# Kernel tuning notes

Measured on AMD Instinct MI355X. Metric: run time of the kernel, lower is better.

The kernel has to match this reference:

```python
import jax, jax.numpy as jnp
import numpy as np

STATE_DIM = 256
MAX_NODES = 64
EPS = 1e-5
EDGE_THRESHOLD = 0.3


def _glorot(key, shape):
    fan_in = shape[0]
    bound = 1.0 / np.sqrt(fan_in)
    return jax.random.uniform(key, shape, jnp.float32, -bound, bound)


def setup_inputs() -> dict:
    key = jax.random.key(0)
    ks = jax.random.split(key, 16)
    D = STATE_DIM
    d2, d4 = D // 2, D // 4
    inp = {
        "state_sequence": jax.random.normal(ks[0], (256, 128, D), jnp.float32),
        # node encoder
        "W1": _glorot(ks[1], (D, d2)), "b1": jnp.zeros((d2,), jnp.float32),
        "W2": _glorot(ks[2], (d2, d4)), "b2": jnp.zeros((d4,), jnp.float32),
        "gamma": jnp.ones((d4,), jnp.float32), "beta": jnp.zeros((d4,), jnp.float32),
        # edge predictor (input dim d2 = 2*d4)
        "E1": _glorot(ks[3], (d2, 64)), "bE1": jnp.zeros((64,), jnp.float32),
        "E2": _glorot(ks[4], (64, 32)), "bE2": jnp.zeros((32,), jnp.float32),
        "E3": _glorot(ks[5], (32, 1)), "bE3": jnp.zeros((1,), jnp.float32),
        # strength estimator
        "S1": _glorot(ks[6], (d2, 32)), "bS1": jnp.zeros((32,), jnp.float32),
        "S2": _glorot(ks[7], (32, 1)), "bS2": jnp.zeros((1,), jnp.float32),
    }
    return inp


def reference(state_sequence, W1, b1, W2, b2, gamma, beta,
              E1, bE1, E2, bE2, E3, bE3, S1, bS1, S2, bS2):
    B, S, D = state_sequence.shape
    N = MAX_NODES
    # pad if seq shorter than max_nodes (static shapes, here S >= N so no-op branch)
    if S < N:
        state_sequence = jnp.pad(state_sequence, ((0, 0), (0, N - S), (0, 0)))
        S = N
    # linspace indices, truncated to long like torch.linspace(..., dtype=long)
    idx = jnp.linspace(0.0, S - 1, N).astype(jnp.int32)
    nodes = state_sequence[:, idx]                      # [B, N, D]

    # node encoder: Linear -> ReLU -> (Dropout eval) -> Linear -> LayerNorm
    h = jax.nn.relu(jnp.einsum('bnd,de->bne', nodes, W1) + b1)
    h = jnp.einsum('bnd,de->bne', h, W2) + b2           # [B, N, D//4]
    mu = jnp.mean(h, axis=-1, keepdims=True)
    var = jnp.mean((h - mu) ** 2, axis=-1, keepdims=True)
    node_features = (h - mu) * jax.lax.rsqrt(var + EPS) * gamma + beta
    node_features = jnp.nan_to_num(node_features, nan=0.0)

    d4 = node_features.shape[-1]
    # pair input is concat([f_i, f_j]); split first-layer weights to avoid
    # materializing the [B,N,N,2*d4] concat tensor.
    # edge predictor first layer
    ei = jnp.einsum('bnd,dh->bnh', node_features, E1[:d4])   # [B, N, 64]
    ej = jnp.einsum('bnd,dh->bnh', node_features, E1[d4:])
    he = jax.nn.relu(ei[:, :, None, :] + ej[:, None, :, :] + bE1)  # [B,N,N,64]
    he = jax.nn.relu(jnp.einsum('bijh,hk->bijk', he, E2) + bE2)    # [B,N,N,32]
    edge_prob = jax.nn.sigmoid(jnp.einsum('bijk,ko->bijo', he, E3) + bE3)[..., 0]

    # strength estimator
    si = jnp.einsum('bnd,dh->bnh', node_features, S1[:d4])
    sj = jnp.einsum('bnd,dh->bnh', node_features, S1[d4:])
    hs = jax.nn.relu(si[:, :, None, :] + sj[:, None, :, :] + bS1)  # [B,N,N,32]
    strength = jnp.tanh(jnp.einsum('bijk,ko->bijo', hs, S2) + bS2)[..., 0]

    offdiag = 1.0 - jnp.eye(N, dtype=edge_prob.dtype)   # i != j only
    adjacency = edge_prob * offdiag
    strengths = strength * offdiag
    adjacency = jnp.where(adjacency > EDGE_THRESHOLD, adjacency, 0.0)
    return node_features, adjacency, strengths
```

## Files before the change

### kernel.cpp

```cpp
#include <hip/hip_runtime.h>
#include <hip/hip_bf16.h>
#include <math.h>

typedef __attribute__((ext_vector_type(8))) short short8;
typedef __attribute__((ext_vector_type(4))) short short4v;
typedef __attribute__((ext_vector_type(4))) float f32x4;
typedef __attribute__((ext_vector_type(2))) _Float16 h2;
typedef __attribute__((ext_vector_type(4))) _Float16 h4;
typedef __attribute__((ext_vector_type(8))) _Float16 h8;

__device__ __forceinline__ short f2bf(float f) {
    __hip_bfloat16 h = __float2bfloat16(f);
    return __builtin_bit_cast(short, h);
}

__global__ __launch_bounds__(256)
void kernelA0(const float* __restrict__ W1, const float* __restrict__ W2,
              const float* __restrict__ E1, const float* __restrict__ S1,
              short* __restrict__ wT)
{
    const int tid = blockIdx.x * 256 + threadIdx.x;
    {
        const int k = tid >> 7, n = tid & 127;
        wT[n * 256 + k] = f2bf(W1[tid]);
    }
    if (tid < 8192) {
        const int k = tid >> 6, n = tid & 63;
        wT[32768 + n * 128 + k] = f2bf(W2[tid]);
    }
    if (tid < 8192) {
        const int rr = tid >> 6, c = tid & 63;
        const int o = (rr < 64) ? c : (64 + c);
        const int k = (rr < 64) ? rr : (rr - 64);
        wT[40960 + o * 64 + k] = f2bf(E1[tid]);
    }
    if (tid < 4096) {
        const int rr = tid >> 5, c = tid & 31;
        const int o = (rr < 64) ? (128 + c) : (160 + c);
        const int k = (rr < 64) ? rr : (rr - 64);
        wT[40960 + o * 64 + k] = f2bf(S1[tid]);
    }
}

constexpr int XS_S  = 264;
constexpr int NH1_S = 136;
constexpr int NHS_S = 68;
constexpr int NNF_S = 72;

__global__ __launch_bounds__(256, 2)
void kernelN(const float* __restrict__ x,
             const float* __restrict__ b1, const float* __restrict__ b2,
             const float* __restrict__ gamma, const float* __restrict__ beta,
             const short* __restrict__ wT,
             const float* __restrict__ bE1, const float* __restrict__ bS1,
             float* __restrict__ out_nf,
             float* __restrict__ ws_ei, float* __restrict__ ws_ej,
             float* __restrict__ ws_si, float* __restrict__ ws_sj)
{
    __shared__ short Xs [16 * XS_S];
    __shared__ short h1B[16 * NH1_S];
    __shared__ float Hs [16 * NHS_S];
    __shared__ short nfB[16 * NNF_S];

    const int t  = threadIdx.x;
    const int rg = blockIdx.x;
    const int b  = blockIdx.y;
    const int w  = t >> 6, l = t & 63, g = l >> 4, r = l & 15;
    const short* W1T = wT;
    const short* W2T = wT + 32768;
    const short* WcT = wT + 40960;

    {
        const int row = t >> 4, c0 = t & 15;
        const int m = 16 * rg + row;
        const int srow = (m == 63) ? 127 : (int)((float)m * (127.0f / 63.0f));
        const float* xrow = x + ((size_t)b * 128 + srow) * 256;
#pragma unroll
        for (int i = 0; i < 4; ++i) {
            const int c4 = (c0 + 16 * i) * 4;
            const float4 v = *(const float4*)(xrow + c4);
            short4v s;
            s[0] = f2bf(v.x); s[1] = f2bf(v.y); s[2] = f2bf(v.z); s[3] = f2bf(v.w);
            *(short4v*)&Xs[row * XS_S + c4] = s;
        }
    }
    __syncthreads();

#pragma unroll
    for (int nt2 = 0; nt2 < 2; ++nt2) {
        const int n = 32 * w + 16 * nt2 + r;
        f32x4 acca = {0.f, 0.f, 0.f, 0.f};
        f32x4 accb = {0.f, 0.f, 0.f, 0.f};
#pragma unroll
        for (int ks = 0; ks < 4; ++ks) {
            const short8 a0  = *(const short8*)&Xs[r * XS_S + 32 * ks + 8 * g];
            const short8 a1  = *(const short8*)&Xs[r * XS_S + 32 * (ks + 4) + 8 * g];
            const short8 bwa = *(const short8*)(W1T + (size_t)n * 256 + 32 * ks + 8 * g);
            const short8 bwb = *(const short8*)(W1T + (size_t)n * 256 + 32 * (ks + 4) + 8 * g);
            acca = __builtin_amdgcn_mfma_f32_16x16x32_bf16(a0, bwa, acca, 0, 0, 0);
            accb = __builtin_amdgcn_mfma_f32_16x16x32_bf16(a1, bwb, accb, 0, 0, 0);
        }
        const float b1v = b1[n];
#pragma unroll
        for (int q = 0; q < 4; ++q)
            h1B[(4 * g + q) * NH1_S + n] = f2bf(fmaxf(acca[q] + accb[q] + b1v, 0.f));
    }
    __syncthreads();

    {
        const int n = 16 * w + r;
        f32x4 acca = {0.f, 0.f, 0.f, 0.f};
        f32x4 accb = {0.f, 0.f, 0.f, 0.f};
#pragma unroll
        for (int ks2 = 0; ks2 < 2; ++ks2) {
            const short8 ha0 = *(const short8*)&h1B[r * NH1_S + 32 * (2 * ks2) + 8 * g];
            const short8 ha1 = *(const short8*)&h1B[r * NH1_S + 32 * (2 * ks2 + 1) + 8 * g];
            const short8 bw0 = *(const short8*)(W2T + (size_t)n * 128 + 32 * (2 * ks2) + 8 * g);
            const short8 bw1 = *(const short8*)(W2T + (size_t)n * 128 + 32 * (2 * ks2 + 1) + 8 * g);
            acca = __builtin_amdgcn_mfma_f32_16x16x32_bf16(ha0, bw0, acca, 0, 0, 0);
            accb = __builtin_amdgcn_mfma_f32_16x16x32_bf16(ha1, bw1, accb, 0, 0, 0);
        }
        const float b2v = b2[n];
#pragma unroll
        for (int q = 0; q < 4; ++q)
            Hs[(4 * g + q) * NHS_S + n] = acca[q] + accb[q] + b2v;
    }
    __syncthreads();

    {
        const int row = t >> 4, c4 = (t & 15) * 4;
        const float4 v = *(const float4*)&Hs[row * NHS_S + c4];
        float s = v.x + v.y + v.z + v.w;
        s += __shfl_xor(s, 1); s += __shfl_xor(s, 2);
        s += __shfl_xor(s, 4); s += __shfl_xor(s, 8);
        const float mu = s * (1.0f / 64.0f);
        float vs = 0.f;
        { const float d0 = v.x-mu, d1 = v.y-mu, d2 = v.z-mu, d3 = v.w-mu;
          vs = fmaf(d0,d0, fmaf(d1,d1, fmaf(d2,d2, d3*d3))); }
        vs += __shfl_xor(vs, 1); vs += __shfl_xor(vs, 2);
        vs += __shfl_xor(vs, 4); vs += __shfl_xor(vs, 8);
        const float rstd = rsqrtf(vs * (1.0f / 64.0f) + 1e-5f);
        const float4 gv = *(const float4*)(gamma + c4);
        const float4 bv = *(const float4*)(beta  + c4);
        float4 o;
        o.x = fmaf((v.x - mu) * rstd, gv.x, bv.x);
        o.y = fmaf((v.y - mu) * rstd, gv.y, bv.y);
        o.z = fmaf((v.z - mu) * rstd, gv.z, bv.z);
        o.w = fmaf((v.w - mu) * rstd, gv.w, bv.w);
        *(float4*)(out_nf + (size_t)b * 4096 + (size_t)(16 * rg + row) * 64 + c4) = o;
        short4v ob;
        ob[0] = f2bf(o.x); ob[1] = f2bf(o.y); ob[2] = f2bf(o.z); ob[3] = f2bf(o.w);
        *(short4v*)&nfB[row * NNF_S + c4] = ob;
    }
    __syncthreads();

    const short8 na0 = *(const short8*)&nfB[r * NNF_S + 8 * g];
    const short8 na1 = *(const short8*)&nfB[r * NNF_S + 32 + 8 * g];
#pragma unroll
    for (int k3 = 0; k3 < 3; ++k3) {
        const int nt = 3 * w + k3;
        const int c = 16 * nt + r;
        const short8 bw0 = *(const short8*)(WcT + (size_t)c * 64 + 8 * g);
        const short8 bw1 = *(const short8*)(WcT + (size_t)c * 64 + 32 + 8 * g);
        f32x4 acc = {0.f, 0.f, 0.f, 0.f};
        acc = __builtin_amdgcn_mfma_f32_16x16x32_bf16(na0, bw0, acc, 0, 0, 0);
        acc = __builtin_amdgcn_mfma_f32_16x16x32_bf16(na1, bw1, acc, 0, 0, 0);
        float* dst; int cc, rs; float badd = 0.f;
        if (nt < 4)       { dst = ws_ei + (size_t)b * 4096; cc = c;       rs = 64; badd = bE1[c]; }
        else if (nt < 8)  { dst = ws_ej + (size_t)b * 4096; cc = c - 64;  rs = 64; }
        else if (nt < 10) { dst = ws_si + (size_t)b * 2048; cc = c - 128; rs = 32; badd = bS1[c - 128]; }
        else              { dst = ws_sj + (size_t)b * 2048; cc = c - 160; rs = 32; }
#pragma unroll
        for (int q = 0; q < 4; ++q)
            dst[(size_t)(16 * rg + 4 * g + q) * rs + cc] = acc[q] + badd;
    }
}

constexpr int EJH = 34;
constexpr int SJH = 18;

__global__ __launch_bounds__(256, 2)
void kernelB(const float* __restrict__ ws_ei, const float* __restrict__ ws_ej,
             const float* __restrict__ ws_si, const float* __restrict__ ws_sj,
             const float* __restrict__ E2,
             const float* __restrict__ bE2, const float* __restrict__ E3,
             const float* __restrict__ bE3,
             const float* __restrict__ S2, const float* __restrict__ bS2,
             float* __restrict__ out_adj, float* __restrict__ out_str)
{
    __shared__ h2 ejH[64 * EJH];
    __shared__ h2 eiH[16 * EJH];
    __shared__ h2 sjH[64 * SJH];
    __shared__ h2 siH[16 * SJH];
    __shared__ float bE2s[32], E3s[32];

    const int t  = threadIdx.x;
    const int qi = blockIdx.x;
    const int b  = blockIdx.y;
    const int w  = t >> 6, l = t & 63;
    const int g  = l >> 4, r = l & 15;

#pragma unroll
    for (int it = 0; it < 8; ++it) {
        const int f = t + 256 * it; const int j = f >> 5, k2 = f & 31;
        const float2 v = *(const float2*)&ws_ej[(size_t)b * 4096 + (size_t)j * 64 + 2 * k2];
        h2 p; p[0] = (_Float16)v.x; p[1] = (_Float16)v.y;
        ejH[j * EJH + k2] = p;
    }
#pragma unroll
    for (int it = 0; it < 2; ++it) {
        const int f = t + 256 * it; const int rr = f >> 5, k2 = f & 31;
        const float2 v = *(const float2*)&ws_ei[(size_t)b * 4096 + (size_t)(qi * 16 + rr) * 64 + 2 * k2];
        h2 p; p[0] = (_Float16)v.x; p[1] = (_Float16)v.y;
        eiH[rr * EJH + k2] = p;
    }
#pragma unroll
    for (int it = 0; it < 4; ++it) {
        const int f = t + 256 * it; const int j = f >> 4, k2 = f & 15;
        const float2 v = *(const float2*)&ws_sj[(size_t)b * 2048 + (size_t)j * 32 + 2 * k2];
        h2 p; p[0] = (_Float16)v.x; p[1] = (_Float16)v.y;
        sjH[j * SJH + k2] = p;
    }
    {
        const int rr = t >> 4, k2 = t & 15;
        const float2 v = *(const float2*)&ws_si[(size_t)b * 2048 + (size_t)(qi * 16 + rr) * 32 + 2 * k2];
        h2 p; p[0] = (_Float16)v.x; p[1] = (_Float16)v.y;
        siH[rr * SJH + k2] = p;
    }
    if (t < 32)      bE2s[t] = bE2[t];
    else if (t < 64) E3s[t - 32] = E3[t - 32];

    h8 aE00, aE10, aE01, aE11;
#pragma unroll
    for (int e = 0; e < 8; ++e) {
        aE00[e] = (_Float16)E2[(size_t)(8 * g + e) * 32 + r];
        aE10[e] = (_Float16)E2[(size_t)(8 * g + e + 32) * 32 + r];
        aE01[e] = (_Float16)E2[(size_t)(8 * g + e) * 32 + r + 16];
        aE11[e] = (_Float16)E2[(size_t)(8 * g + e + 32) * 32 + r + 16];
    }
    const float bE3v = bE3[0], bS2v = bS2[0];
    const h4 z4 = {(_Float16)0.f, (_Float16)0.f, (_Float16)0.f, (_Float16)0.f};
    __syncthreads();

    h4 ei0a[4], ei0b[4], ei1a[4], ei1b[4];
#pragma unroll
    for (int ii = 0; ii < 4; ++ii) {
        const int il = 4 * w + ii;
        ei0a[ii] = *(const h4*)&eiH[il * EJH + 4 * g];
        ei0b[ii] = *(const h4*)&eiH[il * EJH + 4 * g + 2];
        ei1a[ii] = *(const h4*)&eiH[il * EJH + 16 + 4 * g];
        ei1b[ii] = *(const h4*)&eiH[il * EJH + 16 + 4 * g + 2];
    }

    for (int jt = 0; jt < 4; ++jt) {
        const int j = (jt << 4) + r;
        const h4 ej0a = *(const h4*)&ejH[j * EJH + 4 * g];
        const h4 ej0b = *(const h4*)&ejH[j * EJH + 4 * g + 2];
        const h4 ej1a = *(const h4*)&ejH[j * EJH + 16 + 4 * g];
        const h4 ej1b = *(const h4*)&ejH[j * EJH + 16 + 4 * g + 2];

#pragma unroll
        for (int ii = 0; ii < 4; ++ii) {
            const int ig = qi * 16 + 4 * w + ii;

            const h4 he0a = __builtin_elementwise_max(ei0a[ii] + ej0a, z4);
            const h4 he0b = __builtin_elementwise_max(ei0b[ii] + ej0b, z4);
            const h4 he1a = __builtin_elementwise_max(ei1a[ii] + ej1a, z4);
            const h4 he1b = __builtin_elementwise_max(ei1b[ii] + ej1b, z4);
            const h8 b0 = __builtin_shufflevector(he0a, he0b, 0, 1, 2, 3, 4, 5, 6, 7);
            const h8 b1 = __builtin_shufflevector(he1a, he1b, 0, 1, 2, 3, 4, 5, 6, 7);

            f32x4 acc0 = {0.f, 0.f, 0.f, 0.f};
            f32x4 acc1 = {0.f, 0.f, 0.f, 0.f};
            acc0 = __builtin_amdgcn_mfma_f32_16x16x32_f16(aE00, b0, acc0, 0, 0, 0);
            acc0 = __builtin_amdgcn_mfma_f32_16x16x32_f16(aE10, b1, acc0, 0, 0, 0);
            acc1 = __builtin_amdgcn_mfma_f32_16x16x32_f16(aE01, b0, acc1, 0, 0, 0);
            acc1 = __builtin_amdgcn_mfma_f32_16x16x32_f16(aE11, b1, acc1, 0, 0, 0);

            float pe = 0.f;
#pragma unroll
            for (int q = 0; q < 4; ++q) {
                const int k0 = 4 * g + q;
                pe += fmaxf(acc0[q] + bE2s[k0], 0.f) * E3s[k0];
                pe += fmaxf(acc1[q] + bE2s[k0 + 16], 0.f) * E3s[k0 + 16];
            }
            pe += __shfl_xor(pe, 16);
            pe += __shfl_xor(pe, 32);

            if (l < 16) {
                const float z = pe + bE3v;
                const float p = 1.0f / (1.0f + __expf(-z));
                const float av = (j == ig || !(p > 0.3f)) ? 0.f : p;
                out_adj[(size_t)b * 4096 + (size_t)ig * 64 + j] = av;
            }
        }
    }

    {
        h4 s2h[8];
#pragma unroll
        for (int q8 = 0; q8 < 8; ++q8) {
            h4 p;
            p[0] = (_Float16)S2[4 * q8];     p[1] = (_Float16)S2[4 * q8 + 1];
            p[2] = (_Float16)S2[4 * q8 + 2]; p[3] = (_Float16)S2[4 * q8 + 3];
            s2h[q8] = p;
        }
        const int j = t & 63;
        const int ib = (t >> 6) * 4;
        h4 sj4[8];
#pragma unroll
        for (int q8 = 0; q8 < 8; ++q8)
            sj4[q8] = *(const h4*)&sjH[j * SJH + 2 * q8];
#pragma unroll
        for (int ii = 0; ii < 4; ++ii) {
            const int il = ib + ii;
            const int ig = qi * 16 + il;
            float sacc = 0.f;
#pragma unroll
            for (int q8 = 0; q8 < 8; ++q8) {
                const h4 si4 = *(const h4*)&siH[il * SJH + 2 * q8];
                const h4 hs = __builtin_elementwise_max(si4 + sj4[q8], z4);
                const h2 lo   = __builtin_shufflevector(hs, hs, 0, 1);
                const h2 hi   = __builtin_shufflevector(hs, hs, 2, 3);
                const h2 s2lo = __builtin_shufflevector(s2h[q8], s2h[q8], 0, 1);
                const h2 s2hi = __builtin_shufflevector(s2h[q8], s2h[q8], 2, 3);
                sacc = __builtin_amdgcn_fdot2(lo, s2lo, sacc, false);
                sacc = __builtin_amdgcn_fdot2(hi, s2hi, sacc, false);
            }
            const float xs = sacc + bS2v;
            const float e2x = __expf(2.0f * xs);
            const float sv = (j == ig) ? 0.f : (e2x - 1.0f) / (e2x + 1.0f);
            out_str[(size_t)b * 4096 + (size_t)ig * 64 + j] = sv;
        }
    }
}

extern "C" void kernel_launch(void* const* d_in, const int* in_sizes, int n_in,
                              void* d_out, int out_size, void* d_ws, size_t ws_size,
                              hipStream_t stream)
{
    const float* x     = (const float*)d_in[0];
    const float* W1    = (const float*)d_in[1];
    const float* b1    = (const float*)d_in[2];
    const float* W2    = (const float*)d_in[3];
    const float* b2    = (const float*)d_in[4];
    const float* gamma = (const float*)d_in[5];
    const float* beta  = (const float*)d_in[6];
    const float* E1    = (const float*)d_in[7];
    const float* bE1   = (const float*)d_in[8];
    const float* E2    = (const float*)d_in[9];
    const float* bE2   = (const float*)d_in[10];
    const float* E3    = (const float*)d_in[11];
    const float* bE3   = (const float*)d_in[12];
    const float* S1    = (const float*)d_in[13];
    const float* bS1   = (const float*)d_in[14];
    const float* S2    = (const float*)d_in[15];
    const float* bS2   = (const float*)d_in[16];

    float* out     = (float*)d_out;
    float* out_nf  = out;
    float* out_adj = out + 1048576;
    float* out_str = out + 2097152;

    short* wT    = (short*)d_ws;
    float* wsf   = (float*)d_ws;
    float* ws_ei = wsf + 32768;
    float* ws_ej = ws_ei + 1048576;
    float* ws_si = ws_ej + 1048576;
    float* ws_sj = ws_si + 524288;

    kernelA0<<<128, 256, 0, stream>>>(W1, W2, E1, S1, wT);

    kernelN<<<dim3(4, 256), 256, 0, stream>>>(
        x, b1, b2, gamma, beta, wT, bE1, bS1,
        out_nf, ws_ei, ws_ej, ws_si, ws_sj);

    kernelB<<<dim3(4, 256), 256, 0, stream>>>(
        ws_ei, ws_ej, ws_si, ws_sj,
        E2, bE2, E3, bE3, S2, bS2,
        out_adj, out_str);
}
```

Baseline: 45.80 us.

## Fuse node encoder and pairwise edge kernels into one per-batch kernel

Merges the node-encoder kernel and the pairwise edge/strength kernel into a single 1024-thread block per batch element. The ei/ej/si/sj projections are kept in LDS as fp16 instead of being written to and reread from global workspace. This removes one launch and the global round trip of the intermediates. The cost is 256 large blocks with about 68KB of LDS each, which lowers occupancy and parallelism compared with the earlier 1024 smaller blocks.

```diff
diff --git a/kernel.cpp b/kernel.cpp
--- a/kernel.cpp
+++ b/kernel.cpp
@@ -42,38 +42,68 @@
     }
 }
 
-constexpr int XS_S  = 264;
-constexpr int NH1_S = 136;
-constexpr int NHS_S = 68;
+constexpr int XS_S  = 260;
+constexpr int H1B_S = 136;
+constexpr int HS_S  = 68;
 constexpr int NNF_S = 72;
-
-__global__ __launch_bounds__(256, 2)
-void kernelN(const float* __restrict__ x,
+constexpr int EJW   = 68;
+constexpr int SJW   = 36;
+
+constexpr int OFF_XS  = 0;
+constexpr int OFF_EIH = 0;
+constexpr int OFF_EJH = 8704;
+constexpr int OFF_SIH = 17408;
+constexpr int OFF_SJH = 22016;
+constexpr int OFF_H1B = 33280;
+constexpr int OFF_HS  = 50688;
+constexpr int LDS_BYTES = 68096;
+
+__global__ __launch_bounds__(1024)
+void kernelF(const float* __restrict__ x,
              const float* __restrict__ b1, const float* __restrict__ b2,
              const float* __restrict__ gamma, const float* __restrict__ beta,
              const short* __restrict__ wT,
-             const float* __restrict__ bE1, const float* __restrict__ bS1,
-             float* __restrict__ out_nf,
-             float* __restrict__ ws_ei, float* __restrict__ ws_ej,
-             float* __restrict__ ws_si, float* __restrict__ ws_sj)
+             const float* __restrict__ bE1, const float* __restrict__ E2,
+             const float* __restrict__ bE2, const float* __restrict__ E3,
+             const float* __restrict__ bE3, const float* __restrict__ bS1,
+             const float* __restrict__ S2, const float* __restrict__ bS2,
+             float* __restrict__ out_nf, float* __restrict__ out_adj,
+             float* __restrict__ out_str)
 {
-    __shared__ short Xs [16 * XS_S];
-    __shared__ short h1B[16 * NH1_S];
-    __shared__ float Hs [16 * NHS_S];
-    __shared__ short nfB[16 * NNF_S];
-
-    const int t  = threadIdx.x;
-    const int rg = blockIdx.x;
-    const int b  = blockIdx.y;
-    const int w  = t >> 6, l = t & 63, g = l >> 4, r = l & 15;
+    extern __shared__ char lds[];
+    short*    XsS  = (short*)(lds + OFF_XS);
+    short*    h1BS = (short*)(lds + OFF_H1B);
+    float*    HsS  = (float*)(lds + OFF_HS);
+    short*    nfBS = (short*)(lds + OFF_H1B);
+    _Float16* eihS = (_Float16*)(lds + OFF_EIH);
+    _Float16* ejhS = (_Float16*)(lds + OFF_EJH);
+    _Float16* sihS = (_Float16*)(lds + OFF_SIH);
+    _Float16* sjhS = (_Float16*)(lds + OFF_SJH);
+    __shared__ float bE2s[32], E3s[32];
+
+    const int t = threadIdx.x, b = blockIdx.x;
+    const int w = t >> 6, l = t & 63, g = l >> 4, r = l & 15;
     const short* W1T = wT;
     const short* W2T = wT + 32768;
     const short* WcT = wT + 40960;
 
+    if (t < 32)      bE2s[t] = bE2[t];
+    else if (t < 64) E3s[t - 32] = E3[t - 32];
+
+    h8 aE00, aE10, aE01, aE11;
+#pragma unroll
+    for (int e = 0; e < 8; ++e) {
+        aE00[e] = (_Float16)E2[(size_t)(8 * g + e) * 32 + r];
+        aE10[e] = (_Float16)E2[(size_t)(8 * g + e + 32) * 32 + r];
+        aE01[e] = (_Float16)E2[(size_t)(8 * g + e) * 32 + r + 16];
+        aE11[e] = (_Float16)E2[(size_t)(8 * g + e + 32) * 32 + r + 16];
+    }
+    const float bE3v = bE3[0], bS2v = bS2[0];
+    const h4 z4 = {(_Float16)0.f, (_Float16)0.f, (_Float16)0.f, (_Float16)0.f};
+
     {
         const int row = t >> 4, c0 = t & 15;
-        const int m = 16 * rg + row;
-        const int srow = (m == 63) ? 127 : (int)((float)m * (127.0f / 63.0f));
+        const int srow = (row == 63) ? 127 : (int)((float)row * (127.0f / 63.0f));
         const float* xrow = x + ((size_t)b * 128 + srow) * 256;
 #pragma unroll
         for (int i = 0; i < 4; ++i) {
@@ -81,40 +111,46 @@
             const float4 v = *(const float4*)(xrow + c4);
             short4v s;
             s[0] = f2bf(v.x); s[1] = f2bf(v.y); s[2] = f2bf(v.z); s[3] = f2bf(v.w);
-            *(short4v*)&Xs[row * XS_S + c4] = s;
-        }
-    }
-    __syncthreads();
-
-#pragma unroll
-    for (int nt2 = 0; nt2 < 2; ++nt2) {
-        const int n = 32 * w + 16 * nt2 + r;
+            *(short4v*)&XsS[row * XS_S + c4] = s;
+        }
+    }
+    __syncthreads();
+
+    {
+        const int mt = w >> 2, nb = (w & 3) << 1;
+        const int aRow = (16 * mt + r) * XS_S;
+#pragma unroll
+        for (int np = 0; np < 2; ++np) {
+            const int n = ((nb + np) << 4) + r;
+            f32x4 acca = {0.f, 0.f, 0.f, 0.f};
+            f32x4 accb = {0.f, 0.f, 0.f, 0.f};
+#pragma unroll
+            for (int ks = 0; ks < 4; ++ks) {
+                const short8 a0  = *(const short8*)&XsS[aRow + 32 * ks + 8 * g];
+                const short8 a1  = *(const short8*)&XsS[aRow + 32 * (ks + 4) + 8 * g];
+                const short8 bwa = *(const short8*)(W1T + (size_t)n * 256 + 32 * ks + 8 * g);
+                const short8 bwb = *(const short8*)(W1T + (size_t)n * 256 + 32 * (ks + 4) + 8 * g);
+                acca = __builtin_amdgcn_mfma_f32_16x16x32_bf16(a0, bwa, acca, 0, 0, 0);
+                accb = __builtin_amdgcn_mfma_f32_16x16x32_bf16(a1, bwb, accb, 0, 0, 0);
+            }
+            const float b1v = b1[n];
+#pragma unroll
+            for (int q = 0; q < 4; ++q)
+                h1BS[(16 * mt + 4 * g + q) * H1B_S + n] = f2bf(fmaxf(acca[q] + accb[q] + b1v, 0.f));
+        }
+    }
+    __syncthreads();
+
+    {
+        const int mt = w >> 2;
+        const int n = ((w & 3) << 4) + r;
+        const int aRow = (16 * mt + r) * H1B_S;
         f32x4 acca = {0.f, 0.f, 0.f, 0.f};
         f32x4 accb = {0.f, 0.f, 0.f, 0.f};
 #pragma unroll
-        for (int ks = 0; ks < 4; ++ks) {
-            const short8 a0  = *(const short8*)&Xs[r * XS_S + 32 * ks + 8 * g];
-            const short8 a1  = *(const short8*)&Xs[r * XS_S + 32 * (ks + 4) + 8 * g];
-            const short8 bwa = *(const short8*)(W1T + (size_t)n * 256 + 32 * ks + 8 * g);
-            const short8 bwb = *(const short8*)(W1T + (size_t)n * 256 + 32 * (ks + 4) + 8 * g);
-            acca = __builtin_amdgcn_mfma_f32_16x16x32_bf16(a0, bwa, acca, 0, 0, 0);
-            accb = __builtin_amdgcn_mfma_f32_16x16x32_bf16(a1, bwb, accb, 0, 0, 0);
-        }
-        const float b1v = b1[n];
-#pragma unroll
-        for (int q = 0; q < 4; ++q)
-            h1B[(4 * g + q) * NH1_S + n] = f2bf(fmaxf(acca[q] + accb[q] + b1v, 0.f));
-    }
-    __syncthreads();
-
-    {
-        const int n = 16 * w + r;
-        f32x4 acca = {0.f, 0.f, 0.f, 0.f};
-        f32x4 accb = {0.f, 0.f, 0.f, 0.f};
-#pragma unroll
         for (int ks2 = 0; ks2 < 2; ++ks2) {
-            const short8 ha0 = *(const short8*)&h1B[r * NH1_S + 32 * (2 * ks2) + 8 * g];
-            const short8 ha1 = *(const short8*)&h1B[r * NH1_S + 32 * (2 * ks2 + 1) + 8 * g];
+            const short8 ha0 = *(const short8*)&h1BS[aRow + 32 * (2 * ks2) + 8 * g];
+            const short8 ha1 = *(const short8*)&h1BS[aRow + 32 * (2 * ks2 + 1) + 8 * g];
             const short8 bw0 = *(const short8*)(W2T + (size_t)n * 128 + 32 * (2 * ks2) + 8 * g);
             const short8 bw1 = *(const short8*)(W2T + (size_t)n * 128 + 32 * (2 * ks2 + 1) + 8 * g);
             acca = __builtin_amdgcn_mfma_f32_16x16x32_bf16(ha0, bw0, acca, 0, 0, 0);
@@ -123,13 +159,13 @@
         const float b2v = b2[n];
 #pragma unroll
         for (int q = 0; q < 4; ++q)
-            Hs[(4 * g + q) * NHS_S + n] = acca[q] + accb[q] + b2v;
+            HsS[(16 * mt + 4 * g + q) * HS_S + n] = acca[q] + accb[q] + b2v;
     }
     __syncthreads();
 
     {
         const int row = t >> 4, c4 = (t & 15) * 4;
-        const float4 v = *(const float4*)&Hs[row * NHS_S + c4];
+        const float4 v = *(const float4*)&HsS[row * HS_S + c4];
         float s = v.x + v.y + v.z + v.w;
         s += __shfl_xor(s, 1); s += __shfl_xor(s, 2);
         s += __shfl_xor(s, 4); s += __shfl_xor(s, 8);
@@ -147,151 +183,101 @@
         o.y = fmaf((v.y - mu) * rstd, gv.y, bv.y);
         o.z = fmaf((v.z - mu) * rstd, gv.z, bv.z);
         o.w = fmaf((v.w - mu) * rstd, gv.w, bv.w);
-        *(float4*)(out_nf + (size_t)b * 4096 + (size_t)(16 * rg + row) * 64 + c4) = o;
+        *(float4*)(out_nf + (size_t)b * 4096 + (size_t)row * 64 + c4) = o;
         short4v ob;
         ob[0] = f2bf(o.x); ob[1] = f2bf(o.y); ob[2] = f2bf(o.z); ob[3] = f2bf(o.w);
-        *(short4v*)&nfB[row * NNF_S + c4] = ob;
-    }
-    __syncthreads();
-
-    const short8 na0 = *(const short8*)&nfB[r * NNF_S + 8 * g];
-    const short8 na1 = *(const short8*)&nfB[r * NNF_S + 32 + 8 * g];
-#pragma unroll
-    for (int k3 = 0; k3 < 3; ++k3) {
-        const int nt = 3 * w + k3;
-        const int c = 16 * nt + r;
-        const short8 bw0 = *(const short8*)(WcT + (size_t)c * 64 + 8 * g);
-        const short8 bw1 = *(const short8*)(WcT + (size_t)c * 64 + 32 + 8 * g);
-        f32x4 acc = {0.f, 0.f, 0.f, 0.f};
-        acc = __builtin_amdgcn_mfma_f32_16x16x32_bf16(na0, bw0, acc, 0, 0, 0);
-        acc = __builtin_amdgcn_mfma_f32_16x16x32_bf16(na1, bw1, acc, 0, 0, 0);
-        float* dst; int cc, rs; float badd = 0.f;
-        if (nt < 4)       { dst = ws_ei + (size_t)b * 4096; cc = c;       rs = 64; badd = bE1[c]; }
-        else if (nt < 8)  { dst = ws_ej + (size_t)b * 4096; cc = c - 64;  rs = 64; }
-        else if (nt < 10) { dst = ws_si + (size_t)b * 2048; cc = c - 128; rs = 32; badd = bS1[c - 128]; }
-        else              { dst = ws_sj + (size_t)b * 2048; cc = c - 160; rs = 32; }
-#pragma unroll
-        for (int q = 0; q < 4; ++q)
-            dst[(size_t)(16 * rg + 4 * g + q) * rs + cc] = acc[q] + badd;
-    }
-}
-
-constexpr int EJH = 34;
-constexpr int SJH = 18;
-
-__global__ __launch_bounds__(256, 2)
-void kernelB(const float* __restrict__ ws_ei, const float* __restrict__ ws_ej,
-             const float* __restrict__ ws_si, const float* __restrict__ ws_sj,
-             const float* __restrict__ E2,
-             const float* __restrict__ bE2, const float* __restrict__ E3,
-             const float* __restrict__ bE3,
-             const float* __restrict__ S2, const float* __restrict__ bS2,
-             float* __restrict__ out_adj, float* __restrict__ out_str)
-{
-    __shared__ h2 ejH[64 * EJH];
-    __shared__ h2 eiH[16 * EJH];
-    __shared__ h2 sjH[64 * SJH];
-    __shared__ h2 siH[16 * SJH];
-    __shared__ float bE2s[32], E3s[32];
-
-    const int t  = threadIdx.x;
-    const int qi = blockIdx.x;
-    const int b  = blockIdx.y;
-    const int w  = t >> 6, l = t & 63;
-    const int g  = l >> 4, r = l & 15;
-
-#pragma unroll
-    for (int it = 0; it < 8; ++it) {
-        const int f = t + 256 * it; const int j = f >> 5, k2 = f & 31;
-        const float2 v = *(const float2*)&ws_ej[(size_t)b * 4096 + (size_t)j * 64 + 2 * k2];
-        h2 p; p[0] = (_Float16)v.x; p[1] = (_Float16)v.y;
-        ejH[j * EJH + k2] = p;
-    }
-#pragma unroll
-    for (int it = 0; it < 2; ++it) {
-        const int f = t + 256 * it; const int rr = f >> 5, k2 = f & 31;
-        const float2 v = *(const float2*)&ws_ei[(size_t)b * 4096 + (size_t)(qi * 16 + rr) * 64 + 2 * k2];
-        h2 p; p[0] = (_Float16)v.x; p[1] = (_Float16)v.y;
-        eiH[rr * EJH + k2] = p;
-    }
-#pragma unroll
-    for (int it = 0; it < 4; ++it) {
-        const int f = t + 256 * it; const int j = f >> 4, k2 = f & 15;
-        const float2 v = *(const float2*)&ws_sj[(size_t)b * 2048 + (size_t)j * 32 + 2 * k2];
-        h2 p; p[0] = (_Float16)v.x; p[1] = (_Float16)v.y;
-        sjH[j * SJH + k2] = p;
-    }
-    {
-        const int rr = t >> 4, k2 = t & 15;
-        const float2 v = *(const float2*)&ws_si[(size_t)b * 2048 + (size_t)(qi * 16 + rr) * 32 + 2 * k2];
-        h2 p; p[0] = (_Float16)v.x; p[1] = (_Float16)v.y;
-        siH[rr * SJH + k2] = p;
-    }
-    if (t < 32)      bE2s[t] = bE2[t];
-    else if (t < 64) E3s[t - 32] = E3[t - 32];
-
-    h8 aE00, aE10, aE01, aE11;
-#pragma unroll
-    for (int e = 0; e < 8; ++e) {
-        aE00[e] = (_Float16)E2[(size_t)(8 * g + e) * 32 + r];
-        aE10[e] = (_Float16)E2[(size_t)(8 * g + e + 32) * 32 + r];
-        aE01[e] = (_Float16)E2[(size_t)(8 * g + e) * 32 + r + 16];
-        aE11[e] = (_Float16)E2[(size_t)(8 * g + e + 32) * 32 + r + 16];
-    }
-    const float bE3v = bE3[0], bS2v = bS2[0];
-    const h4 z4 = {(_Float16)0.f, (_Float16)0.f, (_Float16)0.f, (_Float16)0.f};
-    __syncthreads();
-
-    h4 ei0a[4], ei0b[4], ei1a[4], ei1b[4];
-#pragma unroll
-    for (int ii = 0; ii < 4; ++ii) {
-        const int il = 4 * w + ii;
-        ei0a[ii] = *(const h4*)&eiH[il * EJH + 4 * g];
-        ei0b[ii] = *(const h4*)&eiH[il * EJH + 4 * g + 2];
-        ei1a[ii] = *(const h4*)&eiH[il * EJH + 16 + 4 * g];
-        ei1b[ii] = *(const h4*)&eiH[il * EJH + 16 + 4 * g + 2];
-    }
-
-    for (int jt = 0; jt < 4; ++jt) {
-        const int j = (jt << 4) + r;
-        const h4 ej0a = *(const h4*)&ejH[j * EJH + 4 * g];
-        const h4 ej0b = *(const h4*)&ejH[j * EJH + 4 * g + 2];
-        const h4 ej1a = *(const h4*)&ejH[j * EJH + 16 + 4 * g];
-        const h4 ej1b = *(const h4*)&ejH[j * EJH + 16 + 4 * g + 2];
-
+        *(short4v*)&nfBS[row * NNF_S + c4] = ob;
+    }
+    __syncthreads();
+
+    {
+        const int mt = w >> 2;
+        const short8 na0 = *(const short8*)&nfBS[(16 * mt + r) * NNF_S + 8 * g];
+        const short8 na1 = *(const short8*)&nfBS[(16 * mt + r) * NNF_S + 32 + 8 * g];
+#pragma unroll
+        for (int k3 = 0; k3 < 3; ++k3) {
+            const int ot = (w & 3) * 3 + k3;
+            const int c = 16 * ot + r;
+            const short8 bw0 = *(const short8*)(WcT + (size_t)c * 64 + 8 * g);
+            const short8 bw1 = *(const short8*)(WcT + (size_t)c * 64 + 32 + 8 * g);
+            f32x4 acc = {0.f, 0.f, 0.f, 0.f};
+            acc = __builtin_amdgcn_mfma_f32_16x16x32_bf16(na0, bw0, acc, 0, 0, 0);
+            acc = __builtin_amdgcn_mfma_f32_16x16x32_bf16(na1, bw1, acc, 0, 0, 0);
+            if (ot < 4) {
+                const float bv = bE1[c];
+#pragma unroll
+                for (int q = 0; q < 4; ++q)
+                    eihS[(16 * mt + 4 * g + q) * EJW + c] = (_Float16)(acc[q] + bv);
+            } else if (ot < 8) {
+#pragma unroll
+                for (int q = 0; q < 4; ++q)
+                    ejhS[(16 * mt + 4 * g + q) * EJW + (c - 64)] = (_Float16)acc[q];
+            } else if (ot < 10) {
+                const float bv = bS1[c - 128];
+#pragma unroll
+                for (int q = 0; q < 4; ++q)
+                    sihS[(16 * mt + 4 * g + q) * SJW + (c - 128)] = (_Float16)(acc[q] + bv);
+            } else {
+#pragma unroll
+                for (int q = 0; q < 4; ++q)
+                    sjhS[(16 * mt + 4 * g + q) * SJW + (c - 160)] = (_Float16)acc[q];
+            }
+        }
+    }
+    __syncthreads();
+
+    {
+        h4 ei0a[4], ei0b[4], ei1a[4], ei1b[4];
 #pragma unroll
         for (int ii = 0; ii < 4; ++ii) {
-            const int ig = qi * 16 + 4 * w + ii;
-
-            const h4 he0a = __builtin_elementwise_max(ei0a[ii] + ej0a, z4);
-            const h4 he0b = __builtin_elementwise_max(ei0b[ii] + ej0b, z4);
-            const h4 he1a = __builtin_elementwise_max(ei1a[ii] + ej1a, z4);
-            const h4 he1b = __builtin_elementwise_max(ei1b[ii] + ej1b, z4);
-            const h8 b0 = __builtin_shufflevector(he0a, he0b, 0, 1, 2, 3, 4, 5, 6, 7);
-            const h8 b1 = __builtin_shufflevector(he1a, he1b, 0, 1, 2, 3, 4, 5, 6, 7);
-
-            f32x4 acc0 = {0.f, 0.f, 0.f, 0.f};
-            f32x4 acc1 = {0.f, 0.f, 0.f, 0.f};
-            acc0 = __builtin_amdgcn_mfma_f32_16x16x32_f16(aE00, b0, acc0, 0, 0, 0);
-            acc0 = __builtin_amdgcn_mfma_f32_16x16x32_f16(aE10, b1, acc0, 0, 0, 0);
-            acc1 = __builtin_amdgcn_mfma_f32_16x16x32_f16(aE01, b0, acc1, 0, 0, 0);
-            acc1 = __builtin_amdgcn_mfma_f32_16x16x32_f16(aE11, b1, acc1, 0, 0, 0);
-
-            float pe = 0.f;
-#pragma unroll
-            for (int q = 0; q < 4; ++q) {
-                const int k0 = 4 * g + q;
-                pe += fmaxf(acc0[q] + bE2s[k0], 0.f) * E3s[k0];
-                pe += fmaxf(acc1[q] + bE2s[k0 + 16], 0.f) * E3s[k0 + 16];
-            }
-            pe += __shfl_xor(pe, 16);
-            pe += __shfl_xor(pe, 32);
-
-            if (l < 16) {
-                const float z = pe + bE3v;
-                const float p = 1.0f / (1.0f + __expf(-z));
-                const float av = (j == ig || !(p > 0.3f)) ? 0.f : p;
-                out_adj[(size_t)b * 4096 + (size_t)ig * 64 + j] = av;
+            const int il = 4 * w + ii;
+            ei0a[ii] = *(const h4*)&eihS[il * EJW + 8 * g];
+            ei0b[ii] = *(const h4*)&eihS[il * EJW + 8 * g + 4];
+            ei1a[ii] = *(const h4*)&eihS[il * EJW + 32 + 8 * g];
+            ei1b[ii] = *(const h4*)&eihS[il * EJW + 32 + 8 * g + 4];
+        }
+
+        for (int jt = 0; jt < 4; ++jt) {
+            const int j = (jt << 4) + r;
+            const h4 ej0a = *(const h4*)&ejhS[j * EJW + 8 * g];
+            const h4 ej0b = *(const h4*)&ejhS[j * EJW + 8 * g + 4];
+            const h4 ej1a = *(const h4*)&ejhS[j * EJW + 32 + 8 * g];
+            const h4 ej1b = *(const h4*)&ejhS[j * EJW + 32 + 8 * g + 4];
+
+#pragma unroll
+            for (int ii = 0; ii < 4; ++ii) {
+                const int ig = 4 * w + ii;
+
+                const h4 he0a = __builtin_elementwise_max(ei0a[ii] + ej0a, z4);
+                const h4 he0b = __builtin_elementwise_max(ei0b[ii] + ej0b, z4);
+                const h4 he1a = __builtin_elementwise_max(ei1a[ii] + ej1a, z4);
+                const h4 he1b = __builtin_elementwise_max(ei1b[ii] + ej1b, z4);
+                const h8 b0 = __builtin_shufflevector(he0a, he0b, 0, 1, 2, 3, 4, 5, 6, 7);
+                const h8 b1 = __builtin_shufflevector(he1a, he1b, 0, 1, 2, 3, 4, 5, 6, 7);
+
+                f32x4 acc0 = {0.f, 0.f, 0.f, 0.f};
+                f32x4 acc1 = {0.f, 0.f, 0.f, 0.f};
+                acc0 = __builtin_amdgcn_mfma_f32_16x16x32_f16(aE00, b0, acc0, 0, 0, 0);
+                acc0 = __builtin_amdgcn_mfma_f32_16x16x32_f16(aE10, b1, acc0, 0, 0, 0);
+                acc1 = __builtin_amdgcn_mfma_f32_16x16x32_f16(aE01, b0, acc1, 0, 0, 0);
+                acc1 = __builtin_amdgcn_mfma_f32_16x16x32_f16(aE11, b1, acc1, 0, 0, 0);
+
+                float pe = 0.f;
+#pragma unroll
+                for (int q = 0; q < 4; ++q) {
+                    const int k0 = 4 * g + q;
+                    pe += fmaxf(acc0[q] + bE2s[k0], 0.f) * E3s[k0];
+                    pe += fmaxf(acc1[q] + bE2s[k0 + 16], 0.f) * E3s[k0 + 16];
+                }
+                pe += __shfl_xor(pe, 16);
+                pe += __shfl_xor(pe, 32);
+
+                if (l < 16) {
+                    const float z = pe + bE3v;
+                    const float p = 1.0f / (1.0f + __expf(-z));
+                    const float av = (j == ig || !(p > 0.3f)) ? 0.f : p;
+                    out_adj[(size_t)b * 4096 + (size_t)ig * 64 + j] = av;
+                }
             }
         }
     }
@@ -310,15 +296,14 @@
         h4 sj4[8];
 #pragma unroll
         for (int q8 = 0; q8 < 8; ++q8)
-            sj4[q8] = *(const h4*)&sjH[j * SJH + 2 * q8];
+            sj4[q8] = *(const h4*)&sjhS[j * SJW + 4 * q8];
 #pragma unroll
         for (int ii = 0; ii < 4; ++ii) {
-            const int il = ib + ii;
-            const int ig = qi * 16 + il;
+            const int ig = ib + ii;
             float sacc = 0.f;
 #pragma unroll
             for (int q8 = 0; q8 < 8; ++q8) {
-                const h4 si4 = *(const h4*)&siH[il * SJH + 2 * q8];
+                const h4 si4 = *(const h4*)&sihS[ig * SJW + 4 * q8];
                 const h4 hs = __builtin_elementwise_max(si4 + sj4[q8], z4);
                 const h2 lo   = __builtin_shufflevector(hs, hs, 0, 1);
                 const h2 hi   = __builtin_shufflevector(hs, hs, 2, 3);
@@ -362,21 +347,15 @@
     float* out_adj = out + 1048576;
     float* out_str = out + 2097152;
 
-    short* wT    = (short*)d_ws;
-    float* wsf   = (float*)d_ws;
-    float* ws_ei = wsf + 32768;
-    float* ws_ej = ws_ei + 1048576;
-    float* ws_si = ws_ej + 1048576;
-    float* ws_sj = ws_si + 524288;
+    short* wT = (short*)d_ws;
+
+    (void)hipFuncSetAttribute((const void*)kernelF,
+        hipFuncAttributeMaxDynamicSharedMemorySize, LDS_BYTES);
 
     kernelA0<<<128, 256, 0, stream>>>(W1, W2, E1, S1, wT);
 
-    kernelN<<<dim3(4, 256), 256, 0, stream>>>(
-        x, b1, b2, gamma, beta, wT, bE1, bS1,
-        out_nf, ws_ei, ws_ej, ws_si, ws_sj);
-
-    kernelB<<<dim3(4, 256), 256, 0, stream>>>(
-        ws_ei, ws_ej, ws_si, ws_sj,
-        E2, bE2, E3, bE3, S2, bS2,
-        out_adj, out_str);
+    kernelF<<<256, 1024, LDS_BYTES, stream>>>(
+        x, b1, b2, gamma, beta, wT,
+        bE1, E2, bE2, E3, bE3, bS1, S2, bS2,
+        out_nf, out_adj, out_str);
 }
```

Measured after the change: 39.02 us. 1.17x faster.
